# Performance work log

Hardware: AMD Instinct MI355X
Metric: run time of the kernel (lower is better)

## Reference

```python
import jax, jax.numpy as jnp
import numpy as np

N = 512      # HiPPO state size
L = 65536    # sequence length
DT = 1e-3    # discretization step
UNROLL = 32  # scan unroll (source uses 128; 32 keeps CPU compile fast, same math)


def _make_hippo(n_state):
    # HiPPO-LegS continuous-time (A, B), as in make_hippo
    n = np.arange(n_state)
    P = np.sqrt(1 + 2 * n)
    A = P[:, None] * P[None, :]
    A = np.tril(A) - np.diag(n)
    B = np.sqrt(2 * n + 1.0)[:, None]
    return -A, B


def _discretize(A, B, step):
    # Bilinear (Tustin) discretization, as in discretize
    I = np.eye(A.shape[0])
    BL = np.linalg.inv(I - step / 2 * A)
    Ab = BL @ (I + step / 2 * A)
    Bb = (BL * step) @ B
    return Ab, Bb


def setup_inputs() -> dict:
    key = jax.random.key(0)
    A, B = _make_hippo(N)            # float64 numpy for stable inverse
    Ab, Bb = _discretize(A, B, DT)
    u = jax.random.normal(key, (L,), dtype=jnp.float32)
    return {
        "u": u,
        "Ab": jnp.asarray(Ab, dtype=jnp.float32),   # [N, N]
        "Bb": jnp.asarray(Bb, dtype=jnp.float32),   # [N, 1]
        "x0": jnp.zeros((N,), dtype=jnp.float32),   # last_x initial state
    }


def reference(u, Ab, Bb, x0):
    # Faithful HiPPO.encode: x_{k+1} = Ab @ x_k + Bb @ u_k, returning the
    # full state trajectory f of shape [L, N] (the scan's stacked outputs).
    b = Bb[:, 0]  # Bb @ u[k, None] == b * u_k

    def step(x, u_k):
        x1 = Ab @ x + b * u_k
        return x1, x1

    _, f = jax.lax.scan(step, x0, u, unroll=UNROLL)
    return f
```

## Files before the change

### kernel.cpp

```cpp
#include <hip/hip_runtime.h>
#include <cstdint>
#include <cstddef>


typedef _Float16 half_t;
typedef _Float16 f16x8 __attribute__((ext_vector_type(8)));
typedef float f32x4 __attribute__((ext_vector_type(4)));

static constexpr int KPAD = 544;
static constexpr size_t MSZ = (size_t)512 * 512;
static constexpr float INV2048 = 1.f / 2048.f;

__device__ inline void split1(float v, half_t& h, half_t& l) {
  h = (half_t)v;
  l = (half_t)((v - (float)h) * 2048.f);
}
__device__ inline void split1r(float v, half_t& h, half_t& l) {
  h = (half_t)v;
  l = (half_t)(v - (float)h);
}

__global__ void init_kernel(float4* __restrict__ zp, const float* __restrict__ Ab,
                            float* __restrict__ V0, const float* __restrict__ x0,
                            half_t* __restrict__ xh) {
  int bid = blockIdx.x, tid = threadIdx.x;
  if (bid < 6656) {
    zp[bid * 256 + tid] = make_float4(0.f, 0.f, 0.f, 0.f);
  } else if (bid < 7680) {
    int i = (bid - 6656) * 256 + tid;
    V0[i] = Ab[i];
  } else {
    xh[tid] = (half_t)x0[tid];
    xh[tid + 256] = (half_t)x0[tid + 256];
  }
}

__global__ void kbuild_kernel(const float* __restrict__ V, const float* __restrict__ b,
                              float* __restrict__ K) {
  int gw = blockIdx.x * 4 + (threadIdx.x >> 6);
  int lane = threadIdx.x & 63;
  int t = gw >> 9, n = gw & 511;
  if (t == 0) { if (lane == 0) K[n] = b[n]; return; }
  const float* row = V + (size_t)(t - 1) * MSZ + (size_t)n * 512;
  float acc = 0.f;
#pragma unroll
  for (int m = 0; m < 512; m += 64) acc += row[m + lane] * b[m + lane];
#pragma unroll
  for (int s = 32; s; s >>= 1) acc += __shfl_down(acc, s, 64);
  if (lane == 0) K[t * 512 + n] = acc;
}

__global__ void wcat_fill_kernel(const float* __restrict__ V, const float* __restrict__ K,
                                 half_t* __restrict__ Wh, half_t* __restrict__ Wl) {
  size_t idx = (size_t)blockIdx.x * 256 + threadIdx.x;
  if (idx >= (size_t)8192 * KPAD) return;
  int row = (int)(idx / KPAD), k = (int)(idx % KPAD);
  int i = row >> 9, n = row & 511;
  float v = 0.f;
  if (k < 512) v = V[(size_t)i * MSZ + (size_t)n * 512 + k];
  else if (k < 528) { int j = k - 512; if (j <= i) v = K[(i - j) * 512 + n]; }
  half_t h, l; split1r(v, h, l);
  Wh[idx] = h; Wl[idx] = l;
}

__global__ void leaf_kernel(const float* __restrict__ u, const float* __restrict__ K,
                            half_t* __restrict__ Z) {
  __shared__ float us[16];
  int c = blockIdx.x, n = threadIdx.x;
  if (n < 16) us[n] = u[c * 16 + n];
  __syncthreads();
  float acc = 0.f;
#pragma unroll
  for (int j = 0; j < 16; ++j) acc += K[(15 - j) * 512 + n] * us[j];
  Z[(size_t)c * 512 + n] = (half_t)acc;
}

__global__ void xtail_kernel(const float* __restrict__ u,
                             half_t* __restrict__ Xh, half_t* __restrict__ Xl) {
  int idx = blockIdx.x * 256 + threadIdx.x;
  int c = idx >> 5, j = idx & 31;
  float v = (j < 16) ? u[c * 16 + j] : 0.f;
  size_t o = (size_t)c * KPAD + 512 + j;
  half_t h, l; split1r(v, h, l);
  Xh[o] = h; Xl[o] = l;
}

__device__ __forceinline__ void sq_body(
    const float* __restrict__ A, const float* __restrict__ B, float* __restrict__ C,
    int bx, int by, int sl,
    half_t* __restrict__ Ash, half_t* __restrict__ Asl,
    half_t* __restrict__ Bsh, half_t* __restrict__ Bsl) {
  int m0 = bx * 64, n0 = by * 64;
  int tid = threadIdx.x, wave = tid >> 6, lane = tid & 63;
  int wm = (wave & 1) * 32, wn = (wave >> 1) * 32;
  f32x4 acc[2][2], accc[2][2];
#pragma unroll
  for (int i = 0; i < 2; ++i)
#pragma unroll
    for (int j = 0; j < 2; ++j) {
      acc[i][j] = (f32x4){0.f, 0.f, 0.f, 0.f};
      accc[i][j] = (f32x4){0.f, 0.f, 0.f, 0.f};
    }
  int rb = tid >> 6, mm = tid & 15, kseg = (tid >> 4) & 3;
  const float* ar = A + (size_t)(m0 + rb * 16 + mm) * 512 + sl * 128 + kseg * 8;
  const float* bc = B + (size_t)(sl * 128 + kseg * 8) * 512 + n0 + rb * 16 + mm;
  float4 a0 = *(const float4*)ar, a1 = *(const float4*)(ar + 4);
  float bv[8];
#pragma unroll
  for (int j = 0; j < 8; ++j) bv[j] = bc[(size_t)j * 512];
#pragma unroll
  for (int kt = 0; kt < 4; ++kt) {
    {
      float aa[8] = {a0.x, a0.y, a0.z, a0.w, a1.x, a1.y, a1.z, a1.w};
      f16x8 hv, lv;
#pragma unroll
      for (int j = 0; j < 8; ++j) { half_t h, l; split1(aa[j], h, l); hv[j] = h; lv[j] = l; }
      *(f16x8*)(Ash + tid * 8) = hv;
      *(f16x8*)(Asl + tid * 8) = lv;
#pragma unroll
      for (int j = 0; j < 8; ++j) { half_t h, l; split1(bv[j], h, l); hv[j] = h; lv[j] = l; }
      *(f16x8*)(Bsh + tid * 8) = hv;
      *(f16x8*)(Bsl + tid * 8) = lv;
    }
    __syncthreads();
    if (kt < 3) {
      a0 = *(const float4*)(ar + (kt + 1) * 32);
      a1 = *(const float4*)(ar + (kt + 1) * 32 + 4);
#pragma unroll
      for (int j = 0; j < 8; ++j) bv[j] = bc[(size_t)((kt + 1) * 32 + j) * 512];
    }
    f16x8 afh[2], afl[2], bfh[2], bfl[2];
#pragma unroll
    for (int i = 0; i < 2; ++i) {
      int ra = (wm >> 4) + i, rbn = (wn >> 4) + i;
      afh[i] = *(const f16x8*)(Ash + ra * 512 + lane * 8);
      afl[i] = *(const f16x8*)(Asl + ra * 512 + lane * 8);
      bfh[i] = *(const f16x8*)(Bsh + rbn * 512 + lane * 8);
      bfl[i] = *(const f16x8*)(Bsl + rbn * 512 + lane * 8);
    }
#pragma unroll
    for (int i = 0; i < 2; ++i)
#pragma unroll
      for (int j = 0; j < 2; ++j) {
        acc[i][j] = __builtin_amdgcn_mfma_f32_16x16x32_f16(afh[i], bfh[j], acc[i][j], 0, 0, 0);
        accc[i][j] = __builtin_amdgcn_mfma_f32_16x16x32_f16(afh[i], bfl[j], accc[i][j], 0, 0, 0);
        accc[i][j] = __builtin_amdgcn_mfma_f32_16x16x32_f16(afl[i], bfh[j], accc[i][j], 0, 0, 0);
      }
    __syncthreads();
  }
  int ml = lane & 15, quad = lane >> 4;
  for (int i = 0; i < 2; ++i)
    for (int j = 0; j < 2; ++j)
      for (int rr = 0; rr < 4; ++rr) {
        int gm = m0 + wm + i * 16 + quad * 4 + rr;
        int gn = n0 + wn + j * 16 + ml;
        atomicAdd(&C[(size_t)gm * 512 + gn], acc[i][j][rr] + accc[i][j][rr] * INV2048);
      }
}

__global__ __launch_bounds__(256)
void gemm_nn512(const float* __restrict__ A, long sA,
                const float* __restrict__ B, long sB,
                float* __restrict__ C, long sC) {
  __shared__ __align__(16) half_t s0[64 * 32], s1[64 * 32], s2[64 * 32], s3[64 * 32];
  int bz = blockIdx.z, bb = bz >> 2, sl = bz & 3;
  sq_body(A + (size_t)bb * sA, B + (size_t)bb * sB, C + (size_t)bb * sC,
          blockIdx.x, blockIdx.y, sl, s0, s1, s2, s3);
}

__device__ __forceinline__ void sweep_body(
    const half_t* __restrict__ A, long ldA, const float* __restrict__ BT,
    const half_t* __restrict__ D, long ldD,
    half_t* __restrict__ Ch, half_t* __restrict__ Cl, long ldC,
    int rScale, int rOff, int doCopy, int M, int bx, int by,
    half_t* __restrict__ Ash, half_t* __restrict__ Bsh, half_t* __restrict__ Bsl) {
  int m0 = bx * 64, n0 = by * 64;
  int tid = threadIdx.x, wave = tid >> 6, lane = tid & 63;
  int wm = (wave & 1) * 32, wn = (wave >> 1) * 32;
  f32x4 acc[2][2], accc[2][2];
#pragma unroll
  for (int i = 0; i < 2; ++i)
#pragma unroll
    for (int j = 0; j < 2; ++j) {
      acc[i][j] = (f32x4){0.f, 0.f, 0.f, 0.f};
      accc[i][j] = (f32x4){0.f, 0.f, 0.f, 0.f};
    }
  int rb = tid >> 6, mm = tid & 15, kseg = (tid >> 4) & 3;
  int arow = m0 + rb * 16 + mm;
  const half_t* ap = A + (size_t)arow * ldA + kseg * 8;
  const float* bp = BT + (size_t)(n0 + rb * 16 + mm) * 512 + kseg * 8;
  f16x8 av = (f16x8){0, 0, 0, 0, 0, 0, 0, 0};
  if (arow < M) av = *(const f16x8*)ap;
  float4 bv0 = *(const float4*)bp;
  float4 bv1 = *(const float4*)(bp + 4);
#pragma unroll
  for (int kt = 0; kt < 16; ++kt) {
    int k0 = kt * 32;
    *(f16x8*)(Ash + tid * 8) = av;
    if (doCopy && k0 >= n0 && k0 < n0 + 64 && arow < M) {
      size_t co = (size_t)(2 * arow) * ldC + k0 + kseg * 8;
      *(f16x8*)(Ch + co) = av;
      if (Cl) *(f16x8*)(Cl + co) = (f16x8){0, 0, 0, 0, 0, 0, 0, 0};
    }
    {
      float bb[8] = {bv0.x, bv0.y, bv0.z, bv0.w, bv1.x, bv1.y, bv1.z, bv1.w};
      f16x8 hv, lv;
#pragma unroll
      for (int j = 0; j < 8; ++j) { half_t h, l; split1(bb[j], h, l); hv[j] = h; lv[j] = l; }
      *(f16x8*)(Bsh + tid * 8) = hv;
      *(f16x8*)(Bsl + tid * 8) = lv;
    }
    __syncthreads();
    if (kt < 15) {
      if (arow < M) av = *(const f16x8*)(ap + (kt + 1) * 32);
      bv0 = *(const float4*)(bp + (kt + 1) * 32);
      bv1 = *(const float4*)(bp + (kt + 1) * 32 + 4);
    }
    f16x8 af[2], bfh[2], bfl[2];
#pragma unroll
    for (int i = 0; i < 2; ++i) {
      af[i] = *(const f16x8*)(Ash + ((wm >> 4) + i) * 512 + lane * 8);
      bfh[i] = *(const f16x8*)(Bsh + ((wn >> 4) + i) * 512 + lane * 8);
      bfl[i] = *(const f16x8*)(Bsl + ((wn >> 4) + i) * 512 + lane * 8);
    }
#pragma unroll
    for (int i = 0; i < 2; ++i)
#pragma unroll
      for (int j = 0; j < 2; ++j) {
        acc[i][j] = __builtin_amdgcn_mfma_f32_16x16x32_f16(af[i], bfh[j], acc[i][j], 0, 0, 0);
        accc[i][j] = __builtin_amdgcn_mfma_f32_16x16x32_f16(af[i], bfl[j], accc[i][j], 0, 0, 0);
      }
    __syncthreads();
  }
  int ml = lane & 15, quad = lane >> 4;
  for (int i = 0; i < 2; ++i)
    for (int j = 0; j < 2; ++j)
      for (int rr = 0; rr < 4; ++rr) {
        int gm = m0 + wm + i * 16 + quad * 4 + rr;
        int gn = n0 + wn + j * 16 + ml;
        if (gm >= M) continue;
        float v = acc[i][j][rr] + accc[i][j][rr] * INV2048;
        if (D) v += (float)D[(size_t)gm * ldD + gn];
        size_t co = ((size_t)gm * rScale + rOff) * ldC + gn;
        if (Cl) { half_t h, l; split1r(v, h, l); Ch[co] = h; Cl[co] = l; }
        else Ch[co] = (half_t)v;
      }
}

__global__ __launch_bounds__(256)
void gemm_nt_sweep(const half_t* __restrict__ A, long ldA,
                   const float* __restrict__ BT,
                   const half_t* __restrict__ D, long ldD,
                   half_t* __restrict__ Ch, half_t* __restrict__ Cl,
                   long ldC, int rScale, int rOff, int doCopy, int M) {
  __shared__ __align__(16) half_t s0[64 * 32], s1[64 * 32], s2[64 * 32];
  sweep_body(A, ldA, BT, D, ldD, Ch, Cl, ldC, rScale, rOff, doCopy, M,
             blockIdx.x, blockIdx.y, s0, s1, s2);
}

__global__ __launch_bounds__(256)
void fused_up(const float* __restrict__ T, float* __restrict__ Tout,
              const half_t* __restrict__ Zin, half_t* __restrict__ Zout, int M) {
  __shared__ __align__(16) half_t s0[64 * 32], s1[64 * 32], s2[64 * 32], s3[64 * 32];
  int bid = blockIdx.x;
  if (bid < 256) {
    sq_body(T, T, Tout, bid & 7, (bid >> 3) & 7, bid >> 6, s0, s1, s2, s3);
  } else {
    int b = bid - 256;
    sweep_body(Zin, 1024L, T, Zin + 512, 1024L, Zout, (half_t*)0, 512L,
               1, 0, 0, M, b >> 3, b & 7, s0, s1, s2);
  }
}

__device__ inline void load_lds16(const half_t* g, half_t* l) {
  __builtin_amdgcn_global_load_lds(
      (const __attribute__((address_space(1))) uint32_t*)g,
      (__attribute__((address_space(3))) uint32_t*)l, 16, 0, 0);
}

__global__ __launch_bounds__(512, 2)
void gemm_main(const half_t* __restrict__ Ah, const half_t* __restrict__ Al,
               const half_t* __restrict__ Bh, const half_t* __restrict__ Bl,
               float* __restrict__ C) {
  __shared__ __align__(16) half_t sm[2 * 4 * 8192];
  int bid = blockIdx.x;
  int xcd = bid & 7, loc = bid >> 3;
  int mt = (xcd & 1) * 8 + (loc >> 3);
  int nt = (xcd >> 1) * 8 + (loc & 7);
  int m0 = mt * 256, n0 = nt * 256;
  int tid = threadIdx.x, wave = tid >> 6, lane = tid & 63;
  int wm = (wave & 1) * 128, wn = (wave >> 1) * 64;
  int mm = lane & 15, kseg = lane >> 4;
  f32x4 acc[8][4];
#pragma unroll
  for (int f = 0; f < 8; ++f)
#pragma unroll
    for (int g = 0; g < 4; ++g) acc[f][g] = (f32x4){0.f, 0.f, 0.f, 0.f};

  const size_t ga0 = (size_t)(m0 + wave * 16 + mm) * KPAD + kseg * 8;
  const size_t gb0 = (size_t)(n0 + wave * 16 + mm) * KPAD + kseg * 8;
  const size_t qstep = (size_t)128 * KPAD;

  auto stage = [&](int nb, int kt, int q) {
    size_t go = (size_t)kt * 32 + (size_t)q * qstep;
    half_t* d = sm + (size_t)nb * 32768 + (size_t)(wave + 8 * q) * 512;
    load_lds16(Ah + ga0 + go, d);
    load_lds16(Al + ga0 + go, d + 8192);
    load_lds16(Bh + gb0 + go, d + 16384);
    load_lds16(Bl + gb0 + go, d + 24576);
  };

  stage(0, 0, 0);
  stage(0, 0, 1);
  asm volatile("s_waitcnt vmcnt(0)" ::: "memory");
  __builtin_amdgcn_s_barrier();

  const int lread = lane * 8;
  const int arow = (wm >> 4);
  const int brow = (wn >> 4);
  for (int kt = 0; kt < 17; ++kt) {
    const int cur = kt & 1;
    const half_t* SA_h = sm + cur * 32768;
    const half_t* SA_l = SA_h + 8192;
    const half_t* SB_h = SA_h + 16384;
    const half_t* SB_l = SA_h + 24576;
    const bool pre = kt < 16;
    f16x8 ah[4], al[4], bh0[2], bl0[2], bh1[2], bl1[2];

#pragma unroll
    for (int i = 0; i < 4; ++i) {
      ah[i] = *(const f16x8*)(SA_h + (arow + i) * 512 + lread);
      al[i] = *(const f16x8*)(SA_l + (arow + i) * 512 + lread);
    }
#pragma unroll
    for (int j = 0; j < 2; ++j) {
      bh0[j] = *(const f16x8*)(SB_h + (brow + j) * 512 + lread);
      bl0[j] = *(const f16x8*)(SB_l + (brow + j) * 512 + lread);
    }
    if (pre) stage(cur ^ 1, kt + 1, 0);
    __builtin_amdgcn_s_barrier();
    asm volatile("s_waitcnt lgkmcnt(0)" ::: "memory");
    __builtin_amdgcn_sched_barrier(0);
    __builtin_amdgcn_s_setprio(1);
#pragma unroll
    for (int i = 0; i < 4; ++i)
#pragma unroll
      for (int j = 0; j < 2; ++j) {
        acc[i][j] = __builtin_amdgcn_mfma_f32_16x16x32_f16(ah[i], bh0[j], acc[i][j], 0, 0, 0);
        acc[i][j] = __builtin_amdgcn_mfma_f32_16x16x32_f16(ah[i], bl0[j], acc[i][j], 0, 0, 0);
        acc[i][j] = __builtin_amdgcn_mfma_f32_16x16x32_f16(al[i], bh0[j], acc[i][j], 0, 0, 0);
      }
    __builtin_amdgcn_s_setprio(0);
    __builtin_amdgcn_s_barrier();

#pragma unroll
    for (int j = 0; j < 2; ++j) {
      bh1[j] = *(const f16x8*)(SB_h + (brow + 2 + j) * 512 + lread);
      bl1[j] = *(const f16x8*)(SB_l + (brow + 2 + j) * 512 + lread);
    }
    if (pre) stage(cur ^ 1, kt + 1, 1);
    __builtin_amdgcn_s_barrier();
    asm volatile("s_waitcnt lgkmcnt(0)" ::: "memory");
    __builtin_amdgcn_sched_barrier(0);
    __builtin_amdgcn_s_setprio(1);
#pragma unroll
    for (int i = 0; i < 4; ++i)
#pragma unroll
      for (int j = 0; j < 2; ++j) {
        acc[i][2 + j] = __builtin_amdgcn_mfma_f32_16x16x32_f16(ah[i], bh1[j], acc[i][2 + j], 0, 0, 0);
        acc[i][2 + j] = __builtin_amdgcn_mfma_f32_16x16x32_f16(ah[i], bl1[j], acc[i][2 + j], 0, 0, 0);
        acc[i][2 + j] = __builtin_amdgcn_mfma_f32_16x16x32_f16(al[i], bh1[j], acc[i][2 + j], 0, 0, 0);
      }
    __builtin_amdgcn_s_setprio(0);
    __builtin_amdgcn_s_barrier();

#pragma unroll
    for (int i = 0; i < 4; ++i) {
      ah[i] = *(const f16x8*)(SA_h + (arow + 4 + i) * 512 + lread);
      al[i] = *(const f16x8*)(SA_l + (arow + 4 + i) * 512 + lread);
    }
    __builtin_amdgcn_s_barrier();
    asm volatile("s_waitcnt lgkmcnt(0)" ::: "memory");
    __builtin_amdgcn_sched_barrier(0);
    __builtin_amdgcn_s_setprio(1);
#pragma unroll
    for (int i = 0; i < 4; ++i)
#pragma unroll
      for (int j = 0; j < 2; ++j) {
        acc[4 + i][2 + j] = __builtin_amdgcn_mfma_f32_16x16x32_f16(ah[i], bh1[j], acc[4 + i][2 + j], 0, 0, 0);
        acc[4 + i][2 + j] = __builtin_amdgcn_mfma_f32_16x16x32_f16(ah[i], bl1[j], acc[4 + i][2 + j], 0, 0, 0);
        acc[4 + i][2 + j] = __builtin_amdgcn_mfma_f32_16x16x32_f16(al[i], bh1[j], acc[4 + i][2 + j], 0, 0, 0);
      }
#pragma unroll
    for (int i = 0; i < 4; ++i)
#pragma unroll
      for (int j = 0; j < 2; ++j) {
        acc[4 + i][j] = __builtin_amdgcn_mfma_f32_16x16x32_f16(ah[i], bh0[j], acc[4 + i][j], 0, 0, 0);
        acc[4 + i][j] = __builtin_amdgcn_mfma_f32_16x16x32_f16(ah[i], bl0[j], acc[4 + i][j], 0, 0, 0);
        acc[4 + i][j] = __builtin_amdgcn_mfma_f32_16x16x32_f16(al[i], bh0[j], acc[4 + i][j], 0, 0, 0);
      }
    __builtin_amdgcn_s_setprio(0);
    asm volatile("s_waitcnt vmcnt(0)" ::: "memory");
    __builtin_amdgcn_s_barrier();
  }

  int ml = lane & 15, quad = lane >> 4;
#pragma unroll
  for (int f = 0; f < 8; ++f)
#pragma unroll
    for (int g = 0; g < 4; ++g) {
      int gm = m0 + wm + f * 16 + quad * 4;
      int gn = n0 + wn + g * 16 + ml;
      float* o = C + (size_t)gm * 8192 + gn;
#pragma unroll
      for (int rr = 0; rr < 4; ++rr)
        o[(size_t)rr * 8192] = acc[f][g][rr];
    }
}


extern "C" void kernel_launch(void* const* d_in, const int* in_sizes, int n_in,
                              void* d_out, int out_size, void* d_ws, size_t ws_size,
                              hipStream_t stream) {
  (void)in_sizes; (void)n_in; (void)out_size; (void)ws_size;
  const float* u  = (const float*)d_in[0];
  const float* Ab = (const float*)d_in[1];
  const float* Bb = (const float*)d_in[2];
  const float* x0 = (const float*)d_in[3];
  float* out = (float*)d_out;

  char* base = (char*)d_ws;
  size_t off = 0;
  auto carve = [&](size_t bytes) -> char* {
    char* p = base + off;
    off = (off + bytes + 255) & ~(size_t)255;
    return p;
  };
  float*  Vp  = (float*)carve(16 * MSZ * 4);
  float*  Sp  = (float*)carve(11 * MSZ * 4);
  float*  Kb  = (float*)carve((size_t)16 * 512 * 4);
  half_t* Wh  = (half_t*)carve((size_t)8192 * KPAD * 2);
  half_t* Wl  = (half_t*)carve((size_t)8192 * KPAD * 2);
  half_t* x0h = (half_t*)carve(512 * 2);
  size_t zoff[13]; zoff[0] = 0;
  for (int l = 0; l < 12; ++l) zoff[l + 1] = zoff[l] + (size_t)(4096 >> l) * 512;
  size_t xoff[13]; xoff[1] = 0;
  for (int l = 1; l < 12; ++l) xoff[l + 1] = xoff[l] + (size_t)(4096 >> l) * 512;
  half_t* Zh  = (half_t*)Vp;
  half_t* Xph = (half_t*)((char*)Vp + ((zoff[12] * 2 + 255) & ~(size_t)255));
  half_t* Xch = (half_t*)Sp;
  half_t* Xcl = (half_t*)((char*)Sp + (((size_t)4096 * KPAD * 2 + 255) & ~(size_t)255));

  hipLaunchKernelGGL(init_kernel, dim3(7681), dim3(256), 0, stream,
                     (float4*)(Vp + MSZ), Ab, Vp, x0, x0h);

  for (int s = 1; s <= 8; s <<= 1) {
    hipLaunchKernelGGL(gemm_nn512, dim3(8, 8, 4 * s), dim3(256), 0, stream,
                       Vp, (long)MSZ,
                       Vp + (size_t)(s - 1) * MSZ, 0L,
                       Vp + (size_t)s * MSZ, (long)MSZ);
  }

  hipLaunchKernelGGL(kbuild_kernel, dim3(2048), dim3(256), 0, stream, Vp, Bb, Kb);
  hipLaunchKernelGGL(wcat_fill_kernel,
                     dim3((unsigned)(((size_t)8192 * KPAD + 255) / 256)), dim3(256), 0, stream,
                     Vp, Kb, Wh, Wl);
  hipLaunchKernelGGL(leaf_kernel, dim3(4096), dim3(512), 0, stream, u, Kb, Zh);

  auto Smat = [&](int l) -> const float* {
    return (l == 0) ? (Vp + 15 * MSZ) : (Sp + (size_t)(l - 1) * MSZ);
  };

  for (int l = 1; l <= 11; ++l) {
    const float* T = (l == 1) ? Vp + 15 * MSZ : Sp + (size_t)(l - 2) * MSZ;
    float* Tout = Sp + (size_t)(l - 1) * MSZ;
    int Mup = 1 << (12 - l);
    int nswp = ((Mup + 63) / 64) * 8;
    hipLaunchKernelGGL(fused_up, dim3(256 + nswp), dim3(256), 0, stream,
                       T, Tout, Zh + zoff[l - 1], Zh + zoff[l], Mup);
  }

  for (int l = 11; l >= 0; --l) {
    int M = 1 << (11 - l);
    const half_t* Xup = (l == 11) ? x0h : Xph + xoff[l + 1];
    half_t* Ch = (l == 0) ? Xch : Xph + xoff[l];
    half_t* Cl = (l == 0) ? Xcl : (half_t*)0;
    long ldC = (l == 0) ? (long)KPAD : 512L;
    if (l == 0) {
      hipLaunchKernelGGL(xtail_kernel, dim3(512), dim3(256), 0, stream, u, Xch, Xcl);
    }
    hipLaunchKernelGGL(gemm_nt_sweep, dim3((unsigned)((M + 63) / 64), 8), dim3(256), 0, stream,
                       Xup, 512L, Smat(l),
                       Zh + zoff[l], 1024L,
                       Ch, Cl, ldC, 2, 1, 1, M);
  }

  hipLaunchKernelGGL(gemm_main, dim3(512), dim3(512), 0, stream, Xch, Xcl, Wh, Wl, out);
}
```

Before: 699.0 us.

## Fuse the preprocessing kernel chain into one cooperative persistent kernel

Replaces the roughly 30 serial launches (init, power squarings, K build, W fill, leaf, up-sweep and down-sweep levels) with a single cooperative kernel. It loops over virtual blocks and separates the stages with grid-wide syncs, removing per-launch overhead and the tail gaps between many small dependent kernels. The grid is capped at 256 blocks, so the larger stages run fewer concurrent blocks, and each grid.sync adds its own cost. The W fill is also vectorized to 8-element chunks, and the multi-kernel path is kept as a fallback.

```diff
diff --git a/kernel.cpp b/kernel.cpp
--- a/kernel.cpp
+++ b/kernel.cpp
@@ -1,6 +1,9 @@
 #include <hip/hip_runtime.h>
+#include <hip/hip_cooperative_groups.h>
 #include <cstdint>
 #include <cstddef>
+
+namespace cg = cooperative_groups;
 
 
 typedef _Float16 half_t;
@@ -19,6 +22,300 @@
   h = (half_t)v;
   l = (half_t)(v - (float)h);
 }
+
+__device__ __forceinline__ void sq_body(
+    const float* __restrict__ A, const float* __restrict__ B, float* __restrict__ C,
+    int bx, int by, int sl,
+    half_t* __restrict__ Ash, half_t* __restrict__ Asl,
+    half_t* __restrict__ Bsh, half_t* __restrict__ Bsl) {
+  int m0 = bx * 64, n0 = by * 64;
+  int tid = threadIdx.x, wave = tid >> 6, lane = tid & 63;
+  int wm = (wave & 1) * 32, wn = (wave >> 1) * 32;
+  f32x4 acc[2][2], accc[2][2];
+#pragma unroll
+  for (int i = 0; i < 2; ++i)
+#pragma unroll
+    for (int j = 0; j < 2; ++j) {
+      acc[i][j] = (f32x4){0.f, 0.f, 0.f, 0.f};
+      accc[i][j] = (f32x4){0.f, 0.f, 0.f, 0.f};
+    }
+  int rb = tid >> 6, mm = tid & 15, kseg = (tid >> 4) & 3;
+  const float* ar = A + (size_t)(m0 + rb * 16 + mm) * 512 + sl * 128 + kseg * 8;
+  const float* bc = B + (size_t)(sl * 128 + kseg * 8) * 512 + n0 + rb * 16 + mm;
+  float4 a0 = *(const float4*)ar, a1 = *(const float4*)(ar + 4);
+  float bv[8];
+#pragma unroll
+  for (int j = 0; j < 8; ++j) bv[j] = bc[(size_t)j * 512];
+#pragma unroll
+  for (int kt = 0; kt < 4; ++kt) {
+    {
+      float aa[8] = {a0.x, a0.y, a0.z, a0.w, a1.x, a1.y, a1.z, a1.w};
+      f16x8 hv, lv;
+#pragma unroll
+      for (int j = 0; j < 8; ++j) { half_t h, l; split1(aa[j], h, l); hv[j] = h; lv[j] = l; }
+      *(f16x8*)(Ash + tid * 8) = hv;
+      *(f16x8*)(Asl + tid * 8) = lv;
+#pragma unroll
+      for (int j = 0; j < 8; ++j) { half_t h, l; split1(bv[j], h, l); hv[j] = h; lv[j] = l; }
+      *(f16x8*)(Bsh + tid * 8) = hv;
+      *(f16x8*)(Bsl + tid * 8) = lv;
+    }
+    __syncthreads();
+    if (kt < 3) {
+      a0 = *(const float4*)(ar + (kt + 1) * 32);
+      a1 = *(const float4*)(ar + (kt + 1) * 32 + 4);
+#pragma unroll
+      for (int j = 0; j < 8; ++j) bv[j] = bc[(size_t)((kt + 1) * 32 + j) * 512];
+    }
+    f16x8 afh[2], afl[2], bfh[2], bfl[2];
+#pragma unroll
+    for (int i = 0; i < 2; ++i) {
+      int ra = (wm >> 4) + i, rbn = (wn >> 4) + i;
+      afh[i] = *(const f16x8*)(Ash + ra * 512 + lane * 8);
+      afl[i] = *(const f16x8*)(Asl + ra * 512 + lane * 8);
+      bfh[i] = *(const f16x8*)(Bsh + rbn * 512 + lane * 8);
+      bfl[i] = *(const f16x8*)(Bsl + rbn * 512 + lane * 8);
+    }
+#pragma unroll
+    for (int i = 0; i < 2; ++i)
+#pragma unroll
+      for (int j = 0; j < 2; ++j) {
+        acc[i][j] = __builtin_amdgcn_mfma_f32_16x16x32_f16(afh[i], bfh[j], acc[i][j], 0, 0, 0);
+        accc[i][j] = __builtin_amdgcn_mfma_f32_16x16x32_f16(afh[i], bfl[j], accc[i][j], 0, 0, 0);
+        accc[i][j] = __builtin_amdgcn_mfma_f32_16x16x32_f16(afl[i], bfh[j], accc[i][j], 0, 0, 0);
+      }
+    __syncthreads();
+  }
+  int ml = lane & 15, quad = lane >> 4;
+  for (int i = 0; i < 2; ++i)
+    for (int j = 0; j < 2; ++j)
+      for (int rr = 0; rr < 4; ++rr) {
+        int gm = m0 + wm + i * 16 + quad * 4 + rr;
+        int gn = n0 + wn + j * 16 + ml;
+        atomicAdd(&C[(size_t)gm * 512 + gn], acc[i][j][rr] + accc[i][j][rr] * INV2048);
+      }
+}
+
+__device__ __forceinline__ void sweep_body(
+    const half_t* __restrict__ A, long ldA, const float* __restrict__ BT,
+    const half_t* __restrict__ D, long ldD,
+    half_t* __restrict__ Ch, half_t* __restrict__ Cl, long ldC,
+    int rScale, int rOff, int doCopy, int M, int bx, int by,
+    half_t* __restrict__ Ash, half_t* __restrict__ Bsh, half_t* __restrict__ Bsl) {
+  int m0 = bx * 64, n0 = by * 64;
+  int tid = threadIdx.x, wave = tid >> 6, lane = tid & 63;
+  int wm = (wave & 1) * 32, wn = (wave >> 1) * 32;
+  f32x4 acc[2][2], accc[2][2];
+#pragma unroll
+  for (int i = 0; i < 2; ++i)
+#pragma unroll
+    for (int j = 0; j < 2; ++j) {
+      acc[i][j] = (f32x4){0.f, 0.f, 0.f, 0.f};
+      accc[i][j] = (f32x4){0.f, 0.f, 0.f, 0.f};
+    }
+  int rb = tid >> 6, mm = tid & 15, kseg = (tid >> 4) & 3;
+  int arow = m0 + rb * 16 + mm;
+  const half_t* ap = A + (size_t)arow * ldA + kseg * 8;
+  const float* bp = BT + (size_t)(n0 + rb * 16 + mm) * 512 + kseg * 8;
+  f16x8 av = (f16x8){0, 0, 0, 0, 0, 0, 0, 0};
+  if (arow < M) av = *(const f16x8*)ap;
+  float4 bv0 = *(const float4*)bp;
+  float4 bv1 = *(const float4*)(bp + 4);
+#pragma unroll
+  for (int kt = 0; kt < 16; ++kt) {
+    int k0 = kt * 32;
+    *(f16x8*)(Ash + tid * 8) = av;
+    if (doCopy && k0 >= n0 && k0 < n0 + 64 && arow < M) {
+      size_t co = (size_t)(2 * arow) * ldC + k0 + kseg * 8;
+      *(f16x8*)(Ch + co) = av;
+      if (Cl) *(f16x8*)(Cl + co) = (f16x8){0, 0, 0, 0, 0, 0, 0, 0};
+    }
+    {
+      float bb[8] = {bv0.x, bv0.y, bv0.z, bv0.w, bv1.x, bv1.y, bv1.z, bv1.w};
+      f16x8 hv, lv;
+#pragma unroll
+      for (int j = 0; j < 8; ++j) { half_t h, l; split1(bb[j], h, l); hv[j] = h; lv[j] = l; }
+      *(f16x8*)(Bsh + tid * 8) = hv;
+      *(f16x8*)(Bsl + tid * 8) = lv;
+    }
+    __syncthreads();
+    if (kt < 15) {
+      if (arow < M) av = *(const f16x8*)(ap + (kt + 1) * 32);
+      bv0 = *(const float4*)(bp + (kt + 1) * 32);
+      bv1 = *(const float4*)(bp + (kt + 1) * 32 + 4);
+    }
+    f16x8 af[2], bfh[2], bfl[2];
+#pragma unroll
+    for (int i = 0; i < 2; ++i) {
+      af[i] = *(const f16x8*)(Ash + ((wm >> 4) + i) * 512 + lane * 8);
+      bfh[i] = *(const f16x8*)(Bsh + ((wn >> 4) + i) * 512 + lane * 8);
+      bfl[i] = *(const f16x8*)(Bsl + ((wn >> 4) + i) * 512 + lane * 8);
+    }
+#pragma unroll
+    for (int i = 0; i < 2; ++i)
+#pragma unroll
+      for (int j = 0; j < 2; ++j) {
+        acc[i][j] = __builtin_amdgcn_mfma_f32_16x16x32_f16(af[i], bfh[j], acc[i][j], 0, 0, 0);
+        accc[i][j] = __builtin_amdgcn_mfma_f32_16x16x32_f16(af[i], bfl[j], accc[i][j], 0, 0, 0);
+      }
+    __syncthreads();
+  }
+  int ml = lane & 15, quad = lane >> 4;
+  for (int i = 0; i < 2; ++i)
+    for (int j = 0; j < 2; ++j)
+      for (int rr = 0; rr < 4; ++rr) {
+        int gm = m0 + wm + i * 16 + quad * 4 + rr;
+        int gn = n0 + wn + j * 16 + ml;
+        if (gm >= M) continue;
+        float v = acc[i][j][rr] + accc[i][j][rr] * INV2048;
+        if (D) v += (float)D[(size_t)gm * ldD + gn];
+        size_t co = ((size_t)gm * rScale + rOff) * ldC + gn;
+        if (Cl) { half_t h, l; split1r(v, h, l); Ch[co] = h; Cl[co] = l; }
+        else Ch[co] = (half_t)v;
+      }
+}
+
+__device__ __forceinline__ size_t zoff_f(int l) {
+  return ((size_t)1 << 22) - ((size_t)1 << (22 - l));
+}
+__device__ __forceinline__ size_t xoff_f(int l) {
+  return ((size_t)1 << 21) - ((size_t)1 << (22 - l));
+}
+
+__global__ __launch_bounds__(256, 2)
+void chain_kernel(const float* __restrict__ u, const float* __restrict__ Ab,
+                  const float* __restrict__ Bb, const float* __restrict__ x0,
+                  float* __restrict__ Vp, float* __restrict__ Sp,
+                  float* __restrict__ Kb, half_t* __restrict__ Wh,
+                  half_t* __restrict__ Wl, half_t* __restrict__ x0h,
+                  half_t* __restrict__ Zh, half_t* __restrict__ Xph,
+                  half_t* __restrict__ Xch, half_t* __restrict__ Xcl) {
+  cg::grid_group grid = cg::this_grid();
+  __shared__ __align__(16) half_t s0[64 * 32], s1[64 * 32], s2[64 * 32], s3[64 * 32];
+  const int bid = blockIdx.x, tid = threadIdx.x;
+  const int G = gridDim.x;
+  auto gsync = [&]() { __threadfence(); grid.sync(); };
+
+  {
+    float4* zp = (float4*)(Vp + MSZ);
+    const int n4 = (int)(26 * MSZ / 4);
+    for (int i = bid * 256 + tid; i < n4; i += G * 256)
+      zp[i] = make_float4(0.f, 0.f, 0.f, 0.f);
+    for (int i = bid * 256 + tid; i < (int)MSZ; i += G * 256) Vp[i] = Ab[i];
+    if (bid == 0) { x0h[tid] = (half_t)x0[tid]; x0h[tid + 256] = (half_t)x0[tid + 256]; }
+  }
+  gsync();
+
+  for (int s = 1; s <= 8; s <<= 1) {
+    for (int vb = bid; vb < 256 * s; vb += G) {
+      int bx = vb & 7, by = (vb >> 3) & 7, z = vb >> 6, bb = z >> 2, sl = z & 3;
+      sq_body(Vp + (size_t)bb * MSZ, Vp + (size_t)(s - 1) * MSZ,
+              Vp + (size_t)(s + bb) * MSZ, bx, by, sl, s0, s1, s2, s3);
+    }
+    gsync();
+  }
+
+  {
+    int wv = tid >> 6, lane = tid & 63;
+    for (int gw = bid * 4 + wv; gw < 8192; gw += G * 4) {
+      int t = gw >> 9, n = gw & 511;
+      if (t == 0) { if (lane == 0) Kb[n] = Bb[n]; continue; }
+      const float* row = Vp + (size_t)(t - 1) * MSZ + (size_t)n * 512;
+      float acc = 0.f;
+#pragma unroll
+      for (int m = 0; m < 512; m += 64) acc += row[m + lane] * Bb[m + lane];
+#pragma unroll
+      for (int sft = 32; sft; sft >>= 1) acc += __shfl_down(acc, sft, 64);
+      if (lane == 0) Kb[t * 512 + n] = acc;
+    }
+  }
+  gsync();
+
+  {
+    for (int un = bid * 256 + tid; un < 8192 * 68; un += G * 256) {
+      int row = un / 68, kb = un - row * 68;
+      int i = row >> 9, n = row & 511;
+      f16x8 hv, lv;
+      if (kb < 64) {
+        const float* vp = Vp + (size_t)i * MSZ + (size_t)n * 512 + kb * 8;
+        float4 v0 = *(const float4*)vp, v1 = *(const float4*)(vp + 4);
+        float vv[8] = {v0.x, v0.y, v0.z, v0.w, v1.x, v1.y, v1.z, v1.w};
+#pragma unroll
+        for (int j = 0; j < 8; ++j) { half_t h, l; split1r(vv[j], h, l); hv[j] = h; lv[j] = l; }
+      } else {
+#pragma unroll
+        for (int j = 0; j < 8; ++j) {
+          int k = kb * 8 + j;
+          float v = 0.f;
+          if (k < 528) { int jj = k - 512; if (jj <= i) v = Kb[(i - jj) * 512 + n]; }
+          half_t h, l; split1r(v, h, l); hv[j] = h; lv[j] = l;
+        }
+      }
+      size_t o = (size_t)row * KPAD + kb * 8;
+      *(f16x8*)(Wh + o) = hv;
+      *(f16x8*)(Wl + o) = lv;
+    }
+  }
+  gsync();
+
+  {
+    for (int e = bid * 256 + tid; e < 4096 * 512; e += G * 256) {
+      int c = e >> 9, n = e & 511;
+      float acc = 0.f;
+#pragma unroll
+      for (int j = 0; j < 16; ++j) acc += Kb[(15 - j) * 512 + n] * u[c * 16 + j];
+      Zh[(size_t)e] = (half_t)acc;
+    }
+  }
+  gsync();
+
+  for (int l = 1; l <= 11; ++l) {
+    const float* T = (l == 1) ? Vp + 15 * MSZ : Sp + (size_t)(l - 2) * MSZ;
+    float* Tout = Sp + (size_t)(l - 1) * MSZ;
+    int Mup = 1 << (12 - l);
+    int ntot = 256 + ((Mup + 63) / 64) * 8;
+    const half_t* Zin = Zh + zoff_f(l - 1);
+    half_t* Zout = Zh + zoff_f(l);
+    for (int vb = bid; vb < ntot; vb += G) {
+      if (vb < 256) {
+        sq_body(T, T, Tout, vb & 7, (vb >> 3) & 7, vb >> 6, s0, s1, s2, s3);
+      } else {
+        int b = vb - 256;
+        sweep_body(Zin, 1024L, T, Zin + 512, 1024L, Zout, (half_t*)0, 512L,
+                   1, 0, 0, Mup, b >> 3, b & 7, s0, s1, s2);
+      }
+    }
+    gsync();
+  }
+
+  for (int l = 11; l >= 1; --l) {
+    int M = 1 << (11 - l);
+    const half_t* Xup = (l == 11) ? x0h : Xph + xoff_f(l + 1);
+    half_t* Ch = Xph + xoff_f(l);
+    const float* Sm = Sp + (size_t)(l - 1) * MSZ;
+    const half_t* Dz = Zh + zoff_f(l);
+    int nb = ((M + 63) / 64) * 8;
+    for (int vb = bid; vb < nb; vb += G)
+      sweep_body(Xup, 512L, Sm, Dz, 1024L, Ch, (half_t*)0, 512L,
+                 2, 1, 1, M, vb >> 3, vb & 7, s0, s1, s2);
+    gsync();
+  }
+
+  {
+    for (int e = bid * 256 + tid; e < 4096 * 32; e += G * 256) {
+      int c = e >> 5, j = e & 31;
+      float v = (j < 16) ? u[c * 16 + j] : 0.f;
+      size_t o = (size_t)c * KPAD + 512 + j;
+      half_t h, l; split1r(v, h, l);
+      Xch[o] = h; Xcl[o] = l;
+    }
+    const half_t* Xup = Xph + xoff_f(1);
+    for (int vb = bid; vb < 256; vb += G)
+      sweep_body(Xup, 512L, Vp + 15 * MSZ, Zh + zoff_f(0), 1024L, Xch, Xcl,
+                 (long)KPAD, 2, 1, 1, 2048, vb >> 3, vb & 7, s0, s1, s2);
+  }
+}
+
 
 __global__ void init_kernel(float4* __restrict__ zp, const float* __restrict__ Ab,
                             float* __restrict__ V0, const float* __restrict__ x0,
@@ -52,15 +349,29 @@
 
 __global__ void wcat_fill_kernel(const float* __restrict__ V, const float* __restrict__ K,
                                  half_t* __restrict__ Wh, half_t* __restrict__ Wl) {
-  size_t idx = (size_t)blockIdx.x * 256 + threadIdx.x;
-  if (idx >= (size_t)8192 * KPAD) return;
-  int row = (int)(idx / KPAD), k = (int)(idx % KPAD);
+  int un = blockIdx.x * 256 + threadIdx.x;
+  if (un >= 8192 * 68) return;
+  int row = un / 68, kb = un - row * 68;
   int i = row >> 9, n = row & 511;
-  float v = 0.f;
-  if (k < 512) v = V[(size_t)i * MSZ + (size_t)n * 512 + k];
-  else if (k < 528) { int j = k - 512; if (j <= i) v = K[(i - j) * 512 + n]; }
-  half_t h, l; split1r(v, h, l);
-  Wh[idx] = h; Wl[idx] = l;
+  f16x8 hv, lv;
+  if (kb < 64) {
+    const float* vp = V + (size_t)i * MSZ + (size_t)n * 512 + kb * 8;
+    float4 v0 = *(const float4*)vp, v1 = *(const float4*)(vp + 4);
+    float vv[8] = {v0.x, v0.y, v0.z, v0.w, v1.x, v1.y, v1.z, v1.w};
+#pragma unroll
+    for (int j = 0; j < 8; ++j) { half_t h, l; split1r(vv[j], h, l); hv[j] = h; lv[j] = l; }
+  } else {
+#pragma unroll
+    for (int j = 0; j < 8; ++j) {
+      int k = kb * 8 + j;
+      float v = 0.f;
+      if (k < 528) { int jj = k - 512; if (jj <= i) v = K[(i - jj) * 512 + n]; }
+      half_t h, l; split1r(v, h, l); hv[j] = h; lv[j] = l;
+    }
+  }
+  size_t o = (size_t)row * KPAD + kb * 8;
+  *(f16x8*)(Wh + o) = hv;
+  *(f16x8*)(Wl + o) = lv;
 }
 
 __global__ void leaf_kernel(const float* __restrict__ u, const float* __restrict__ K,
@@ -85,79 +396,6 @@
   Xh[o] = h; Xl[o] = l;
 }
 
-__device__ __forceinline__ void sq_body(
-    const float* __restrict__ A, const float* __restrict__ B, float* __restrict__ C,
-    int bx, int by, int sl,
-    half_t* __restrict__ Ash, half_t* __restrict__ Asl,
-    half_t* __restrict__ Bsh, half_t* __restrict__ Bsl) {
-  int m0 = bx * 64, n0 = by * 64;
-  int tid = threadIdx.x, wave = tid >> 6, lane = tid & 63;
-  int wm = (wave & 1) * 32, wn = (wave >> 1) * 32;
-  f32x4 acc[2][2], accc[2][2];
-#pragma unroll
-  for (int i = 0; i < 2; ++i)
-#pragma unroll
-    for (int j = 0; j < 2; ++j) {
-      acc[i][j] = (f32x4){0.f, 0.f, 0.f, 0.f};
-      accc[i][j] = (f32x4){0.f, 0.f, 0.f, 0.f};
-    }
-  int rb = tid >> 6, mm = tid & 15, kseg = (tid >> 4) & 3;
-  const float* ar = A + (size_t)(m0 + rb * 16 + mm) * 512 + sl * 128 + kseg * 8;
-  const float* bc = B + (size_t)(sl * 128 + kseg * 8) * 512 + n0 + rb * 16 + mm;
-  float4 a0 = *(const float4*)ar, a1 = *(const float4*)(ar + 4);
-  float bv[8];
-#pragma unroll
-  for (int j = 0; j < 8; ++j) bv[j] = bc[(size_t)j * 512];
-#pragma unroll
-  for (int kt = 0; kt < 4; ++kt) {
-    {
-      float aa[8] = {a0.x, a0.y, a0.z, a0.w, a1.x, a1.y, a1.z, a1.w};
-      f16x8 hv, lv;
-#pragma unroll
-      for (int j = 0; j < 8; ++j) { half_t h, l; split1(aa[j], h, l); hv[j] = h; lv[j] = l; }
-      *(f16x8*)(Ash + tid * 8) = hv;
-      *(f16x8*)(Asl + tid * 8) = lv;
-#pragma unroll
-      for (int j = 0; j < 8; ++j) { half_t h, l; split1(bv[j], h, l); hv[j] = h; lv[j] = l; }
-      *(f16x8*)(Bsh + tid * 8) = hv;
-      *(f16x8*)(Bsl + tid * 8) = lv;
-    }
-    __syncthreads();
-    if (kt < 3) {
-      a0 = *(const float4*)(ar + (kt + 1) * 32);
-      a1 = *(const float4*)(ar + (kt + 1) * 32 + 4);
-#pragma unroll
-      for (int j = 0; j < 8; ++j) bv[j] = bc[(size_t)((kt + 1) * 32 + j) * 512];
-    }
-    f16x8 afh[2], afl[2], bfh[2], bfl[2];
-#pragma unroll
-    for (int i = 0; i < 2; ++i) {
-      int ra = (wm >> 4) + i, rbn = (wn >> 4) + i;
-      afh[i] = *(const f16x8*)(Ash + ra * 512 + lane * 8);
-      afl[i] = *(const f16x8*)(Asl + ra * 512 + lane * 8);
-      bfh[i] = *(const f16x8*)(Bsh + rbn * 512 + lane * 8);
-      bfl[i] = *(const f16x8*)(Bsl + rbn * 512 + lane * 8);
-    }
-#pragma unroll
-    for (int i = 0; i < 2; ++i)
-#pragma unroll
-      for (int j = 0; j < 2; ++j) {
-        acc[i][j] = __builtin_amdgcn_mfma_f32_16x16x32_f16(afh[i], bfh[j], acc[i][j], 0, 0, 0);
-        accc[i][j] = __builtin_amdgcn_mfma_f32_16x16x32_f16(afh[i], bfl[j], accc[i][j], 0, 0, 0);
-        accc[i][j] = __builtin_amdgcn_mfma_f32_16x16x32_f16(afl[i], bfh[j], accc[i][j], 0, 0, 0);
-      }
-    __syncthreads();
-  }
-  int ml = lane & 15, quad = lane >> 4;
-  for (int i = 0; i < 2; ++i)
-    for (int j = 0; j < 2; ++j)
-      for (int rr = 0; rr < 4; ++rr) {
-        int gm = m0 + wm + i * 16 + quad * 4 + rr;
-        int gn = n0 + wn + j * 16 + ml;
-        atomicAdd(&C[(size_t)gm * 512 + gn], acc[i][j][rr] + accc[i][j][rr] * INV2048);
-      }
-}
-
 __global__ __launch_bounds__(256)
 void gemm_nn512(const float* __restrict__ A, long sA,
                 const float* __restrict__ B, long sB,
@@ -166,85 +404,6 @@
   int bz = blockIdx.z, bb = bz >> 2, sl = bz & 3;
   sq_body(A + (size_t)bb * sA, B + (size_t)bb * sB, C + (size_t)bb * sC,
           blockIdx.x, blockIdx.y, sl, s0, s1, s2, s3);
-}
-
-__device__ __forceinline__ void sweep_body(
-    const half_t* __restrict__ A, long ldA, const float* __restrict__ BT,
-    const half_t* __restrict__ D, long ldD,
-    half_t* __restrict__ Ch, half_t* __restrict__ Cl, long ldC,
-    int rScale, int rOff, int doCopy, int M, int bx, int by,
-    half_t* __restrict__ Ash, half_t* __restrict__ Bsh, half_t* __restrict__ Bsl) {
-  int m0 = bx * 64, n0 = by * 64;
-  int tid = threadIdx.x, wave = tid >> 6, lane = tid & 63;
-  int wm = (wave & 1) * 32, wn = (wave >> 1) * 32;
-  f32x4 acc[2][2], accc[2][2];
-#pragma unroll
-  for (int i = 0; i < 2; ++i)
-#pragma unroll
-    for (int j = 0; j < 2; ++j) {
-      acc[i][j] = (f32x4){0.f, 0.f, 0.f, 0.f};
-      accc[i][j] = (f32x4){0.f, 0.f, 0.f, 0.f};
-    }
-  int rb = tid >> 6, mm = tid & 15, kseg = (tid >> 4) & 3;
-  int arow = m0 + rb * 16 + mm;
-  const half_t* ap = A + (size_t)arow * ldA + kseg * 8;
-  const float* bp = BT + (size_t)(n0 + rb * 16 + mm) * 512 + kseg * 8;
-  f16x8 av = (f16x8){0, 0, 0, 0, 0, 0, 0, 0};
-  if (arow < M) av = *(const f16x8*)ap;
-  float4 bv0 = *(const float4*)bp;
-  float4 bv1 = *(const float4*)(bp + 4);
-#pragma unroll
-  for (int kt = 0; kt < 16; ++kt) {
-    int k0 = kt * 32;
-    *(f16x8*)(Ash + tid * 8) = av;
-    if (doCopy && k0 >= n0 && k0 < n0 + 64 && arow < M) {
-      size_t co = (size_t)(2 * arow) * ldC + k0 + kseg * 8;
-      *(f16x8*)(Ch + co) = av;
-      if (Cl) *(f16x8*)(Cl + co) = (f16x8){0, 0, 0, 0, 0, 0, 0, 0};
-    }
-    {
-      float bb[8] = {bv0.x, bv0.y, bv0.z, bv0.w, bv1.x, bv1.y, bv1.z, bv1.w};
-      f16x8 hv, lv;
-#pragma unroll
-      for (int j = 0; j < 8; ++j) { half_t h, l; split1(bb[j], h, l); hv[j] = h; lv[j] = l; }
-      *(f16x8*)(Bsh + tid * 8) = hv;
-      *(f16x8*)(Bsl + tid * 8) = lv;
-    }
-    __syncthreads();
-    if (kt < 15) {
-      if (arow < M) av = *(const f16x8*)(ap + (kt + 1) * 32);
-      bv0 = *(const float4*)(bp + (kt + 1) * 32);
-      bv1 = *(const float4*)(bp + (kt + 1) * 32 + 4);
-    }
-    f16x8 af[2], bfh[2], bfl[2];
-#pragma unroll
-    for (int i = 0; i < 2; ++i) {
-      af[i] = *(const f16x8*)(Ash + ((wm >> 4) + i) * 512 + lane * 8);
-      bfh[i] = *(const f16x8*)(Bsh + ((wn >> 4) + i) * 512 + lane * 8);
-      bfl[i] = *(const f16x8*)(Bsl + ((wn >> 4) + i) * 512 + lane * 8);
-    }
-#pragma unroll
-    for (int i = 0; i < 2; ++i)
-#pragma unroll
-      for (int j = 0; j < 2; ++j) {
-        acc[i][j] = __builtin_amdgcn_mfma_f32_16x16x32_f16(af[i], bfh[j], acc[i][j], 0, 0, 0);
-        accc[i][j] = __builtin_amdgcn_mfma_f32_16x16x32_f16(af[i], bfl[j], accc[i][j], 0, 0, 0);
-      }
-    __syncthreads();
-  }
-  int ml = lane & 15, quad = lane >> 4;
-  for (int i = 0; i < 2; ++i)
-    for (int j = 0; j < 2; ++j)
-      for (int rr = 0; rr < 4; ++rr) {
-        int gm = m0 + wm + i * 16 + quad * 4 + rr;
-        int gn = n0 + wn + j * 16 + ml;
-        if (gm >= M) continue;
-        float v = acc[i][j][rr] + accc[i][j][rr] * INV2048;
-        if (D) v += (float)D[(size_t)gm * ldD + gn];
-        size_t co = ((size_t)gm * rScale + rOff) * ldC + gn;
-        if (Cl) { half_t h, l; split1r(v, h, l); Ch[co] = h; Cl[co] = l; }
-        else Ch[co] = (half_t)v;
-      }
 }
 
 __global__ __launch_bounds__(256)
@@ -451,48 +610,66 @@
   half_t* Xch = (half_t*)Sp;
   half_t* Xcl = (half_t*)((char*)Sp + (((size_t)4096 * KPAD * 2 + 255) & ~(size_t)255));
 
-  hipLaunchKernelGGL(init_kernel, dim3(7681), dim3(256), 0, stream,
-                     (float4*)(Vp + MSZ), Ab, Vp, x0, x0h);
-
-  for (int s = 1; s <= 8; s <<= 1) {
-    hipLaunchKernelGGL(gemm_nn512, dim3(8, 8, 4 * s), dim3(256), 0, stream,
-                       Vp, (long)MSZ,
-                       Vp + (size_t)(s - 1) * MSZ, 0L,
-                       Vp + (size_t)s * MSZ, (long)MSZ);
-  }
-
-  hipLaunchKernelGGL(kbuild_kernel, dim3(2048), dim3(256), 0, stream, Vp, Bb, Kb);
-  hipLaunchKernelGGL(wcat_fill_kernel,
-                     dim3((unsigned)(((size_t)8192 * KPAD + 255) / 256)), dim3(256), 0, stream,
-                     Vp, Kb, Wh, Wl);
-  hipLaunchKernelGGL(leaf_kernel, dim3(4096), dim3(512), 0, stream, u, Kb, Zh);
-
-  auto Smat = [&](int l) -> const float* {
-    return (l == 0) ? (Vp + 15 * MSZ) : (Sp + (size_t)(l - 1) * MSZ);
-  };
-
-  for (int l = 1; l <= 11; ++l) {
-    const float* T = (l == 1) ? Vp + 15 * MSZ : Sp + (size_t)(l - 2) * MSZ;
-    float* Tout = Sp + (size_t)(l - 1) * MSZ;
-    int Mup = 1 << (12 - l);
-    int nswp = ((Mup + 63) / 64) * 8;
-    hipLaunchKernelGGL(fused_up, dim3(256 + nswp), dim3(256), 0, stream,
-                       T, Tout, Zh + zoff[l - 1], Zh + zoff[l], Mup);
-  }
-
-  for (int l = 11; l >= 0; --l) {
-    int M = 1 << (11 - l);
-    const half_t* Xup = (l == 11) ? x0h : Xph + xoff[l + 1];
-    half_t* Ch = (l == 0) ? Xch : Xph + xoff[l];
-    half_t* Cl = (l == 0) ? Xcl : (half_t*)0;
-    long ldC = (l == 0) ? (long)KPAD : 512L;
-    if (l == 0) {
-      hipLaunchKernelGGL(xtail_kernel, dim3(512), dim3(256), 0, stream, u, Xch, Xcl);
-    }
-    hipLaunchKernelGGL(gemm_nt_sweep, dim3((unsigned)((M + 63) / 64), 8), dim3(256), 0, stream,
-                       Xup, 512L, Smat(l),
-                       Zh + zoff[l], 1024L,
-                       Ch, Cl, ldC, 2, 1, 1, M);
+  bool coop_done = false;
+  {
+    int dev = 0;
+    (void)hipGetDevice(&dev);
+    int coopAttr = 0;
+    (void)hipDeviceGetAttribute(&coopAttr, hipDeviceAttributeCooperativeLaunch, dev);
+    int ncu = 0;
+    (void)hipDeviceGetAttribute(&ncu, hipDeviceAttributeMultiprocessorCount, dev);
+    int maxb = 0;
+    (void)hipOccupancyMaxActiveBlocksPerMultiprocessor(&maxb, (const void*)chain_kernel, 256, 0);
+    long cap = (long)maxb * (long)ncu;
+    int G = cap < 256 ? (int)cap : 256;
+    if (coopAttr && G >= 64) {
+      void* kargs[] = {(void*)&u, (void*)&Ab, (void*)&Bb, (void*)&x0,
+                       (void*)&Vp, (void*)&Sp, (void*)&Kb, (void*)&Wh, (void*)&Wl,
+                       (void*)&x0h, (void*)&Zh, (void*)&Xph, (void*)&Xch, (void*)&Xcl};
+      hipError_t ce = hipLaunchCooperativeKernel((const void*)chain_kernel,
+                                                 dim3(G), dim3(256), kargs, 0, stream);
+      coop_done = (ce == hipSuccess);
+    }
+  }
+
+  if (!coop_done) {
+    hipLaunchKernelGGL(init_kernel, dim3(7681), dim3(256), 0, stream,
+                       (float4*)(Vp + MSZ), Ab, Vp, x0, x0h);
+    for (int s = 1; s <= 8; s <<= 1) {
+      hipLaunchKernelGGL(gemm_nn512, dim3(8, 8, 4 * s), dim3(256), 0, stream,
+                         Vp, (long)MSZ,
+                         Vp + (size_t)(s - 1) * MSZ, 0L,
+                         Vp + (size_t)s * MSZ, (long)MSZ);
+    }
+    hipLaunchKernelGGL(kbuild_kernel, dim3(2048), dim3(256), 0, stream, Vp, Bb, Kb);
+    hipLaunchKernelGGL(wcat_fill_kernel, dim3(2176), dim3(256), 0, stream,
+                       Vp, Kb, Wh, Wl);
+    hipLaunchKernelGGL(leaf_kernel, dim3(4096), dim3(512), 0, stream, u, Kb, Zh);
+    for (int l = 1; l <= 11; ++l) {
+      const float* T = (l == 1) ? Vp + 15 * MSZ : Sp + (size_t)(l - 2) * MSZ;
+      float* Tout = Sp + (size_t)(l - 1) * MSZ;
+      int Mup = 1 << (12 - l);
+      int nswp = ((Mup + 63) / 64) * 8;
+      hipLaunchKernelGGL(fused_up, dim3(256 + nswp), dim3(256), 0, stream,
+                         T, Tout, Zh + zoff[l - 1], Zh + zoff[l], Mup);
+    }
+    auto Smat = [&](int l) -> const float* {
+      return (l == 0) ? (Vp + 15 * MSZ) : (Sp + (size_t)(l - 1) * MSZ);
+    };
+    for (int l = 11; l >= 0; --l) {
+      int M = 1 << (11 - l);
+      const half_t* Xup = (l == 11) ? x0h : Xph + xoff[l + 1];
+      half_t* Ch = (l == 0) ? Xch : Xph + xoff[l];
+      half_t* Cl = (l == 0) ? Xcl : (half_t*)0;
+      long ldC = (l == 0) ? (long)KPAD : 512L;
+      if (l == 0) {
+        hipLaunchKernelGGL(xtail_kernel, dim3(512), dim3(256), 0, stream, u, Xch, Xcl);
+      }
+      hipLaunchKernelGGL(gemm_nt_sweep, dim3((unsigned)((M + 63) / 64), 8), dim3(256), 0, stream,
+                         Xup, 512L, Smat(l),
+                         Zh + zoff[l], 1024L,
+                         Ch, Cl, ldC, 2, 1, 1, M);
+    }
   }
 
   hipLaunchKernelGGL(gemm_main, dim3(512), dim3(512), 0, stream, Xch, Xcl, Wh, Wl, out);
```

Result: slower. 2.111 ms (+202.0%).
